# Performance work log

Measured on AMD Instinct MI355X. Metric: run time of the kernel, lower is better.

## Reference

```python
import jax, jax.numpy as jnp
import numpy as np

PATCH = 16


def setup_inputs() -> dict:
    key = jax.random.key(0)
    x = jax.random.normal(key, (256, 3, 224, 224), dtype=jnp.float32)
    return {"x": x}


def reference(x):
    P = PATCH
    B, C, Hi, Wi = x.shape
    h, w = Hi // P, Wi // P  # grid rows (h) and cols (w)
    # 'b c (h p1) (w p2) -> b w h p1 p2 c'
    patches = x.reshape(B, C, h, P, w, P).transpose(0, 4, 2, 3, 5, 1)  # (B, w, h, p1, p2, C)
    # center_rotate: transpose p1<->p2 for patches with grid col j in [w/3, 2w/3]
    # and grid row k in [h/3, 2h/3] (original skips j < W/3 or j > 2W/3, same for k)
    jw = jnp.arange(w)
    kh = jnp.arange(h)
    mw = (jw >= w / 3) & (jw <= 2 * w / 3)
    mh = (kh >= h / 3) & (kh <= 2 * h / 3)
    mask = (mw[:, None] & mh[None, :])[None, :, :, None, None, None]  # (1, w, h, 1, 1, 1)
    rot = jnp.where(mask, jnp.swapaxes(patches, 3, 4), patches)  # (B, w, h, a3, a4, C)
    # 'b w h p2 p1 c -> b c (h p2) (w p1)': axis3 is read as p2 (inner height),
    # axis4 as p1 (inner width) -- i.e. every patch gets transposed on reassembly,
    # so center patches (transposed twice) come back in original orientation.
    out = rot.transpose(0, 5, 2, 3, 1, 4).reshape(B, C, h * P, w * P)
    return out
```

## Files before the change

kernel.cpp:

```cpp
#include <hip/hip_runtime.h>


#define WW 224
#define W4 56
#define PP 16
#define NSTRIP_F4 (PP * W4)
#define LDS_S 81

__global__ __launch_bounds__(256) void patch_rotate_kernel(
    const float* __restrict__ x, float* __restrict__ out) {
  const int bid = blockIdx.x;
  const int k  = bid % 14;
  const int bc = bid / 14;
  const int stripBase = (bc * WW + k * PP) * WW;
  const float4* __restrict__ xs = (const float4*)(x + stripBase);
  float4* __restrict__ os = (float4*)(out + stripBase);
  const int tid = threadIdx.x;

  if (k < 5 || k > 9) {
    for (int i = tid; i < NSTRIP_F4; i += 256) os[i] = xs[i];
    return;
  }

  __shared__ float ldsT[PP * LDS_S];

  for (int i = tid; i < PP * 20; i += 256) {
    const int ar = i / 20;
    const int c4 = i % 20;
    const float4 v = xs[ar * W4 + 20 + c4];
    const int jl  = c4 >> 2;
    const int ac0 = (c4 & 3) << 2;
    const int cb  = jl * PP + ar;
    ldsT[(ac0 + 0) * LDS_S + cb] = v.x;
    ldsT[(ac0 + 1) * LDS_S + cb] = v.y;
    ldsT[(ac0 + 2) * LDS_S + cb] = v.z;
    ldsT[(ac0 + 3) * LDS_S + cb] = v.w;
  }

  for (int i = tid; i < PP * 36; i += 256) {
    const int r  = i / 36;
    const int cc = i % 36;
    const int c4 = cc < 20 ? cc : cc + 20;
    os[r * W4 + c4] = xs[r * W4 + c4];
  }

  __syncthreads();

  for (int i = tid; i < PP * 20; i += 256) {
    const int a3 = i / 20;
    const int c4 = i % 20;
    const float* row = ldsT + a3 * LDS_S + c4 * 4;
    float4 v;
    v.x = row[0]; v.y = row[1]; v.z = row[2]; v.w = row[3];
    os[a3 * W4 + 20 + c4] = v;
  }
}

extern "C" void kernel_launch(void* const* d_in, const int* in_sizes, int n_in,
                              void* d_out, int out_size, void* d_ws, size_t ws_size,
                              hipStream_t stream) {
  const float* x = (const float*)d_in[0];
  float* out = (float*)d_out;
  const int blocks = 768 * 14;
  patch_rotate_kernel<<<blocks, 256, 0, stream>>>(x, out);
}
```

Measured before the change: 262.6 us.

## Process one whole image channel per block instead of one row strip

Switches the grid from 768*14 strip blocks of 256 threads to 768 blocks of 512 threads, where each block handles a full 224x224 channel plane. The plain-copy rows and the five centre strips are handled in one block, and the LDS transpose buffer grows to cover all 5x5 centre patches, with the row stride changed to 84. This cuts block count and launch/scheduling overhead, but leaves only 768 blocks on a GPU with many CUs. That means less parallelism and more LDS per block, which could lower occupancy.

Measured after the change: 275.4 us. +4.9%, slower.

```diff
diff --git a/kernel.cpp b/kernel.cpp
--- a/kernel.cpp
+++ b/kernel.cpp
@@ -1,58 +1,54 @@
 #include <hip/hip_runtime.h>
 
 
-#define WW 224
 #define W4 56
-#define PP 16
-#define NSTRIP_F4 (PP * W4)
-#define LDS_S 81
+#define IMG_F4 12544
+#define LDS_S 84
+#define NT 512
 
-__global__ __launch_bounds__(256) void patch_rotate_kernel(
-    const float* __restrict__ x, float* __restrict__ out) {
-  const int bid = blockIdx.x;
-  const int k  = bid % 14;
-  const int bc = bid / 14;
-  const int stripBase = (bc * WW + k * PP) * WW;
-  const float4* __restrict__ xs = (const float4*)(x + stripBase);
-  float4* __restrict__ os = (float4*)(out + stripBase);
+__global__ __launch_bounds__(NT) void patch_rotate_kernel(
+    const float4* __restrict__ x, float4* __restrict__ out) {
+  const int bc = blockIdx.x;
+  const float4* __restrict__ xs = x + (size_t)bc * IMG_F4;
+  float4* __restrict__ os = out + (size_t)bc * IMG_F4;
   const int tid = threadIdx.x;
 
-  if (k < 5 || k > 9) {
-    for (int i = tid; i < NSTRIP_F4; i += 256) os[i] = xs[i];
-    return;
+  __shared__ float ldsT[5 * 16 * LDS_S];
+
+  for (int i = tid; i < 1600; i += NT) {
+    const int sr = i / 20;
+    const int c4 = i % 20;
+    const float4 v = xs[(80 + sr) * W4 + 20 + c4];
+    const int ks = sr >> 4;
+    const int ar = sr & 15;
+    const int jl = c4 >> 2;
+    const int ac0 = (c4 & 3) << 2;
+    float* p = ldsT + (ks * 16 + ac0) * LDS_S + jl * 16 + ar;
+    p[0 * LDS_S] = v.x;
+    p[1 * LDS_S] = v.y;
+    p[2 * LDS_S] = v.z;
+    p[3 * LDS_S] = v.w;
   }
 
-  __shared__ float ldsT[PP * LDS_S];
-
-  for (int i = tid; i < PP * 20; i += 256) {
-    const int ar = i / 20;
-    const int c4 = i % 20;
-    const float4 v = xs[ar * W4 + 20 + c4];
-    const int jl  = c4 >> 2;
-    const int ac0 = (c4 & 3) << 2;
-    const int cb  = jl * PP + ar;
-    ldsT[(ac0 + 0) * LDS_S + cb] = v.x;
-    ldsT[(ac0 + 1) * LDS_S + cb] = v.y;
-    ldsT[(ac0 + 2) * LDS_S + cb] = v.z;
-    ldsT[(ac0 + 3) * LDS_S + cb] = v.w;
-  }
-
-  for (int i = tid; i < PP * 36; i += 256) {
-    const int r  = i / 36;
+  for (int i = tid; i < 4480; i += NT) os[i] = xs[i];
+  for (int i = 8960 + tid; i < IMG_F4; i += NT) os[i] = xs[i];
+  for (int i = tid; i < 2880; i += NT) {
+    const int r = i / 36;
     const int cc = i % 36;
     const int c4 = cc < 20 ? cc : cc + 20;
-    os[r * W4 + c4] = xs[r * W4 + c4];
+    const int idx = (80 + r) * W4 + c4;
+    os[idx] = xs[idx];
   }
 
   __syncthreads();
 
-  for (int i = tid; i < PP * 20; i += 256) {
-    const int a3 = i / 20;
+  for (int i = tid; i < 1600; i += NT) {
+    const int orr = i / 20;
     const int c4 = i % 20;
-    const float* row = ldsT + a3 * LDS_S + c4 * 4;
+    const float* p = ldsT + orr * LDS_S + c4 * 4;
     float4 v;
-    v.x = row[0]; v.y = row[1]; v.z = row[2]; v.w = row[3];
-    os[a3 * W4 + 20 + c4] = v;
+    v.x = p[0]; v.y = p[1]; v.z = p[2]; v.w = p[3];
+    os[(80 + orr) * W4 + 20 + c4] = v;
   }
 }
 
@@ -61,6 +57,5 @@
                               hipStream_t stream) {
   const float* x = (const float*)d_in[0];
   float* out = (float*)d_out;
-  const int blocks = 768 * 14;
-  patch_rotate_kernel<<<blocks, 256, 0, stream>>>(x, out);
+  patch_rotate_kernel<<<768, NT, 0, stream>>>((const float4*)x, (float4*)out);
 }
```
